# Kernel optimization log

Measured on AMD Instinct MI355X. Metric: run time of the kernel, lower is better.

The kernel has to match this reference:

```python
import jax, jax.numpy as jnp
import numpy as np

NEG_SLOPE = 0.2
EPS = 1e-6


def setup_inputs() -> dict:
    key = jax.random.key(0)
    k1, k2 = jax.random.split(key)
    B, C, N = 4, 64, 32768
    x = jax.random.normal(k1, (B, C, 3, N), dtype=jnp.float32)
    # VNLinear weight: nn.Linear(in, out, bias=False).weight -> [out, in]
    W = jax.random.normal(k2, (C, C), dtype=jnp.float32) * (1.0 / np.sqrt(C))
    return {"x": x, "W": W}


def reference(x, W):
    # VNLinear: kron(W, eye(3)) conv2d == per-3-vector channel mix
    # d[b,o,v,n] = sum_i W[o,i] * x[b,i,v,n]
    d = jnp.einsum('oi,bivn->bovn', W, x)
    dotprod = jnp.sum(x * d, axis=2, keepdims=True)      # [B,C,1,N]
    d_norm_sq = jnp.sum(d * d, axis=2, keepdims=True)    # [B,C,1,N]
    neg = x - (1.0 - NEG_SLOPE) * (dotprod / (d_norm_sq + EPS)) * d
    return jnp.where(dotprod >= 0, x, neg)
```

## Files before the change

kernel.cpp:

```cpp
#include <hip/hip_runtime.h>

#define NEG_SLOPE 0.2f
#define EPS 1e-6f


#define C_CH 64
#define V_DIM 3
#define N_FULL 32768
#define NT 64
#define THREADS 512

typedef __attribute__((ext_vector_type(8))) short bf16x8;
typedef __attribute__((ext_vector_type(4))) float f32x4;

__device__ __forceinline__ ushort f2bf(float f) {
    union { float f; unsigned u; } v; v.f = f;
    unsigned r = v.u + 0x7FFFu + ((v.u >> 16) & 1u);
    return (ushort)(r >> 16);
}
__device__ __forceinline__ float bf2f(ushort s) {
    union { unsigned u; float f; } v; v.u = ((unsigned)s) << 16; return v.f;
}
__device__ __forceinline__ unsigned pack_hl(float x) {
    union { float f; unsigned u; } a; a.f = x;
    unsigned t0 = a.u + 0x8000u;
    union { unsigned u; float f; } hb; hb.u = t0 & 0xffff0000u;
    union { float f; unsigned u; } rb; rb.f = x - hb.f;
    return __builtin_amdgcn_perm(t0, rb.u, 0x07060302u);
}
__device__ __forceinline__ float u2f(unsigned u) {
    union { unsigned u; float f; } v; v.u = u; return v.f;
}

__device__ __forceinline__ int swz(int row) { return ((row >> 3) & 3) << 4; }

__global__ __launch_bounds__(THREADS, 4)
void vn_mfma64(const float* __restrict__ x,
               const float* __restrict__ Wf,
               float* __restrict__ out) {
    __shared__ unsigned xs[V_DIM * C_CH][NT];

    const int t    = threadIdx.x;
    const int tile = blockIdx.x;
    const int b    = tile >> 9;
    const int n0   = (tile & 511) << 6;

    const float* xb = x + (size_t)b * (C_CH * V_DIM * N_FULL) + n0;

    const int lane = t & 63;
    const int w    = t >> 6;
    const int wo   = w >> 2;
    const int wn   = w & 3;
    const int l4   = lane & 15;
    const int hi   = lane >> 4;

    float4 xr[6];
    #pragma unroll
    for (int it = 0; it < 6; ++it) {
        int idx = t + it * THREADS;
        int r   = idx >> 4;
        int c4  = (idx & 15) << 2;
        xr[it] = *(const float4*)(xb + (size_t)r * N_FULL + c4);
    }

    bf16x8 Ah[2][2], Al[2][2];
    #pragma unroll
    for (int m = 0; m < 2; ++m)
        #pragma unroll
        for (int kh = 0; kh < 2; ++kh) {
            const float* wp = Wf + (size_t)(wo * 32 + m * 16 + l4) * C_CH + kh * 32 + hi * 8;
            float4 wa = *(const float4*)wp;
            float4 wb = *(const float4*)(wp + 4);
            float wf[8] = {wa.x, wa.y, wa.z, wa.w, wb.x, wb.y, wb.z, wb.w};
            bf16x8 h, l;
            #pragma unroll
            for (int j = 0; j < 8; ++j) {
                ushort hb = f2bf(wf[j]);
                h[j] = (short)hb;
                l[j] = (short)f2bf(wf[j] - bf2f(hb));
            }
            Ah[m][kh] = h; Al[m][kh] = l;
        }

    #pragma unroll
    for (int it = 0; it < 6; ++it) {
        int idx = t + it * THREADS;
        int r   = idx >> 4;
        int c4  = (idx & 15) << 2;
        int i   = (r * 171) >> 9;
        int v   = r - 3 * i;
        int rowp = v * 64 + i;
        unsigned p[4] = {pack_hl(xr[it].x), pack_hl(xr[it].y),
                         pack_hl(xr[it].z), pack_hl(xr[it].w)};
        *(uint4*)&xs[rowp][c4 ^ swz(rowp)] = *(const uint4*)p;
    }
    __syncthreads();

    f32x4 acc[2][3];
    #pragma unroll
    for (int m = 0; m < 2; ++m)
        #pragma unroll
        for (int v = 0; v < 3; ++v)
            acc[m][v] = (f32x4){0.f, 0.f, 0.f, 0.f};

    const int acol = (wn * 16 + l4) ^ (hi << 4);
    #pragma unroll
    for (int v = 0; v < 3; ++v) {
        #pragma unroll
        for (int kh = 0; kh < 2; ++kh) {
            const int rowb = v * 64 + kh * 32 + hi * 8;
            unsigned p[8];
            #pragma unroll
            for (int j = 0; j < 8; ++j)
                p[j] = xs[rowb + j][acol];
            union { bf16x8 v8; unsigned d[4]; } BH, BL;
            #pragma unroll
            for (int q = 0; q < 4; ++q) {
                BH.d[q] = __builtin_amdgcn_perm(p[2 * q + 1], p[2 * q], 0x07060302u);
                BL.d[q] = __builtin_amdgcn_perm(p[2 * q + 1], p[2 * q], 0x05040100u);
            }
            #pragma unroll
            for (int m = 0; m < 2; ++m) {
                acc[m][v] = __builtin_amdgcn_mfma_f32_16x16x32_bf16(Ah[m][kh], BH.v8, acc[m][v], 0, 0, 0);
                acc[m][v] = __builtin_amdgcn_mfma_f32_16x16x32_bf16(Ah[m][kh], BL.v8, acc[m][v], 0, 0, 0);
                acc[m][v] = __builtin_amdgcn_mfma_f32_16x16x32_bf16(Al[m][kh], BH.v8, acc[m][v], 0, 0, 0);
            }
        }
    }

    const int n = wn * 16 + l4;
    float* ob = out + (size_t)b * (C_CH * V_DIM * N_FULL) + n0 + n;
    #pragma unroll
    for (int m = 0; m < 2; ++m) {
        #pragma unroll
        for (int r = 0; r < 4; ++r) {
            const int o = wo * 32 + m * 16 + hi * 4 + r;
            const int ecol = n ^ (((m * 2 + (hi >> 1)) & 3) << 4);
            float xv[3], dv[3];
            #pragma unroll
            for (int v = 0; v < 3; ++v) {
                unsigned p = xs[v * 64 + o][ecol];
                xv[v] = u2f(p & 0xffff0000u) + u2f(p << 16);
                dv[v] = acc[m][v][r];
            }
            float dot  = xv[0] * dv[0] + xv[1] * dv[1] + xv[2] * dv[2];
            float dnsq = dv[0] * dv[0] + dv[1] * dv[1] + dv[2] * dv[2];
            float f = (1.0f - NEG_SLOPE) * dot * __builtin_amdgcn_rcpf(dnsq + EPS);
            f = (dot >= 0.f) ? 0.f : f;
            float o0 = fmaf(-f, dv[0], xv[0]);
            float o1 = fmaf(-f, dv[1], xv[1]);
            float o2 = fmaf(-f, dv[2], xv[2]);
            float* op = ob + (size_t)o * (V_DIM * N_FULL);
            op[0 * N_FULL] = o0;
            op[1 * N_FULL] = o1;
            op[2 * N_FULL] = o2;
        }
    }
}

extern "C" void kernel_launch(void* const* d_in, const int* in_sizes, int n_in,
                              void* d_out, int out_size, void* d_ws, size_t ws_size,
                              hipStream_t stream) {
    const float* x = (const float*)d_in[0];
    const float* W = (const float*)d_in[1];
    float* out = (float*)d_out;

    const int B = 4;
    const int blocks = B * (N_FULL / NT);
    vn_mfma64<<<blocks, THREADS, 0, stream>>>(x, W, out);
}
```

Before: 42.76 us.

## Process four tiles per block with double-buffered LDS and register prefetch

Each block now walks four 32-column tiles with 256 threads. The next tile's global loads are issued into registers before the current tile's MFMA and epilogue, then packed into a second LDS buffer, so load latency overlaps compute. The aim is to hide memory latency and amortise the W split across tiles. The cost is double LDS use, fewer blocks (1024 versus 2048), narrower 128-byte row segments per load, and a lower occupancy hint.

```diff
diff --git a/kernel.cpp b/kernel.cpp
--- a/kernel.cpp
+++ b/kernel.cpp
@@ -7,8 +7,9 @@
 #define C_CH 64
 #define V_DIM 3
 #define N_FULL 32768
-#define NT 64
-#define THREADS 512
+#define NT 32
+#define THREADS 256
+#define TPB 4
 
 typedef __attribute__((ext_vector_type(8))) short bf16x8;
 typedef __attribute__((ext_vector_type(4))) float f32x4;
@@ -32,35 +33,36 @@
     union { unsigned u; float f; } v; v.u = u; return v.f;
 }
 
-__device__ __forceinline__ int swz(int row) { return ((row >> 3) & 3) << 4; }
-
-__global__ __launch_bounds__(THREADS, 4)
-void vn_mfma64(const float* __restrict__ x,
-               const float* __restrict__ Wf,
-               float* __restrict__ out) {
-    __shared__ unsigned xs[V_DIM * C_CH][NT];
-
-    const int t    = threadIdx.x;
-    const int tile = blockIdx.x;
-    const int b    = tile >> 9;
-    const int n0   = (tile & 511) << 6;
-
-    const float* xb = x + (size_t)b * (C_CH * V_DIM * N_FULL) + n0;
+__device__ __forceinline__ int swz(int row) { return ((row >> 3) & 1) << 4; }
+
+__global__ __launch_bounds__(THREADS, 3)
+void vn_pipe(const float* __restrict__ x,
+             const float* __restrict__ Wf,
+             float* __restrict__ out) {
+    __shared__ unsigned xs[2][V_DIM * C_CH][NT];
+
+    const int t     = threadIdx.x;
+    const int tile0 = blockIdx.x * TPB;
+    const int b     = tile0 >> 10;
+    const float* xbase = x   + (size_t)b * (C_CH * V_DIM * N_FULL);
+    float*       obase = out + (size_t)b * (C_CH * V_DIM * N_FULL);
 
     const int lane = t & 63;
     const int w    = t >> 6;
-    const int wo   = w >> 2;
-    const int wn   = w & 3;
+    const int wo   = w >> 1;
+    const int wn   = w & 1;
     const int l4   = lane & 15;
     const int hi   = lane >> 4;
 
+
     float4 xr[6];
-    #pragma unroll
-    for (int it = 0; it < 6; ++it) {
-        int idx = t + it * THREADS;
-        int r   = idx >> 4;
-        int c4  = (idx & 15) << 2;
-        xr[it] = *(const float4*)(xb + (size_t)r * N_FULL + c4);
+    {
+        const float* xb = xbase + ((tile0 & 1023) << 5);
+        #pragma unroll
+        for (int it = 0; it < 6; ++it) {
+            int idx = t + it * THREADS;
+            xr[it] = *(const float4*)(xb + (size_t)(idx >> 3) * N_FULL + ((idx & 7) << 2));
+        }
     }
 
     bf16x8 Ah[2][2], Al[2][2];
@@ -85,76 +87,108 @@
     #pragma unroll
     for (int it = 0; it < 6; ++it) {
         int idx = t + it * THREADS;
-        int r   = idx >> 4;
-        int c4  = (idx & 15) << 2;
+        int r   = idx >> 3;
+        int c4  = (idx & 7) << 2;
         int i   = (r * 171) >> 9;
         int v   = r - 3 * i;
         int rowp = v * 64 + i;
         unsigned p[4] = {pack_hl(xr[it].x), pack_hl(xr[it].y),
                          pack_hl(xr[it].z), pack_hl(xr[it].w)};
-        *(uint4*)&xs[rowp][c4 ^ swz(rowp)] = *(const uint4*)p;
+        *(uint4*)&xs[0][rowp][c4 ^ swz(rowp)] = *(const uint4*)p;
     }
     __syncthreads();
 
-    f32x4 acc[2][3];
+    const int acol = (wn * 16 + l4) ^ ((hi & 1) << 4);
+    const int n    = wn * 16 + l4;
+    const int ecol = n ^ ((hi >> 1) << 4);
+
     #pragma unroll
-    for (int m = 0; m < 2; ++m)
-        #pragma unroll
-        for (int v = 0; v < 3; ++v)
-            acc[m][v] = (f32x4){0.f, 0.f, 0.f, 0.f};
-
-    const int acol = (wn * 16 + l4) ^ (hi << 4);
-    #pragma unroll
-    for (int v = 0; v < 3; ++v) {
-        #pragma unroll
-        for (int kh = 0; kh < 2; ++kh) {
-            const int rowb = v * 64 + kh * 32 + hi * 8;
-            unsigned p[8];
-            #pragma unroll
-            for (int j = 0; j < 8; ++j)
-                p[j] = xs[rowb + j][acol];
-            union { bf16x8 v8; unsigned d[4]; } BH, BL;
-            #pragma unroll
-            for (int q = 0; q < 4; ++q) {
-                BH.d[q] = __builtin_amdgcn_perm(p[2 * q + 1], p[2 * q], 0x07060302u);
-                BL.d[q] = __builtin_amdgcn_perm(p[2 * q + 1], p[2 * q], 0x05040100u);
-            }
-            #pragma unroll
-            for (int m = 0; m < 2; ++m) {
-                acc[m][v] = __builtin_amdgcn_mfma_f32_16x16x32_bf16(Ah[m][kh], BH.v8, acc[m][v], 0, 0, 0);
-                acc[m][v] = __builtin_amdgcn_mfma_f32_16x16x32_bf16(Ah[m][kh], BL.v8, acc[m][v], 0, 0, 0);
-                acc[m][v] = __builtin_amdgcn_mfma_f32_16x16x32_bf16(Al[m][kh], BH.v8, acc[m][v], 0, 0, 0);
-            }
-        }
-    }
-
-    const int n = wn * 16 + l4;
-    float* ob = out + (size_t)b * (C_CH * V_DIM * N_FULL) + n0 + n;
-    #pragma unroll
-    for (int m = 0; m < 2; ++m) {
-        #pragma unroll
-        for (int r = 0; r < 4; ++r) {
-            const int o = wo * 32 + m * 16 + hi * 4 + r;
-            const int ecol = n ^ (((m * 2 + (hi >> 1)) & 3) << 4);
-            float xv[3], dv[3];
-            #pragma unroll
-            for (int v = 0; v < 3; ++v) {
-                unsigned p = xs[v * 64 + o][ecol];
-                xv[v] = u2f(p & 0xffff0000u) + u2f(p << 16);
-                dv[v] = acc[m][v][r];
-            }
-            float dot  = xv[0] * dv[0] + xv[1] * dv[1] + xv[2] * dv[2];
-            float dnsq = dv[0] * dv[0] + dv[1] * dv[1] + dv[2] * dv[2];
-            float f = (1.0f - NEG_SLOPE) * dot * __builtin_amdgcn_rcpf(dnsq + EPS);
-            f = (dot >= 0.f) ? 0.f : f;
-            float o0 = fmaf(-f, dv[0], xv[0]);
-            float o1 = fmaf(-f, dv[1], xv[1]);
-            float o2 = fmaf(-f, dv[2], xv[2]);
-            float* op = ob + (size_t)o * (V_DIM * N_FULL);
-            op[0 * N_FULL] = o0;
-            op[1 * N_FULL] = o1;
-            op[2 * N_FULL] = o2;
-        }
+    for (int tt = 0; tt < TPB; ++tt) {
+        const int cur = tt & 1;
+        const int n0c = ((tile0 + tt) & 1023) << 5;
+
+        if (tt + 1 < TPB) {
+            const float* xb = xbase + (((tile0 + tt + 1) & 1023) << 5);
+            #pragma unroll
+            for (int it = 0; it < 6; ++it) {
+                int idx = t + it * THREADS;
+                xr[it] = *(const float4*)(xb + (size_t)(idx >> 3) * N_FULL + ((idx & 7) << 2));
+            }
+        }
+
+        f32x4 acc[2][3];
+        #pragma unroll
+        for (int m = 0; m < 2; ++m)
+            #pragma unroll
+            for (int v = 0; v < 3; ++v)
+                acc[m][v] = (f32x4){0.f, 0.f, 0.f, 0.f};
+
+        #pragma unroll
+        for (int v = 0; v < 3; ++v) {
+            #pragma unroll
+            for (int kh = 0; kh < 2; ++kh) {
+                const int rowb = v * 64 + kh * 32 + hi * 8;
+                unsigned p[8];
+                #pragma unroll
+                for (int j = 0; j < 8; ++j)
+                    p[j] = xs[cur][rowb + j][acol];
+                union { bf16x8 v8; unsigned d[4]; } BH, BL;
+                #pragma unroll
+                for (int q = 0; q < 4; ++q) {
+                    BH.d[q] = __builtin_amdgcn_perm(p[2 * q + 1], p[2 * q], 0x07060302u);
+                    BL.d[q] = __builtin_amdgcn_perm(p[2 * q + 1], p[2 * q], 0x05040100u);
+                }
+                #pragma unroll
+                for (int m = 0; m < 2; ++m) {
+                    acc[m][v] = __builtin_amdgcn_mfma_f32_16x16x32_bf16(Ah[m][kh], BH.v8, acc[m][v], 0, 0, 0);
+                    acc[m][v] = __builtin_amdgcn_mfma_f32_16x16x32_bf16(Ah[m][kh], BL.v8, acc[m][v], 0, 0, 0);
+                    acc[m][v] = __builtin_amdgcn_mfma_f32_16x16x32_bf16(Al[m][kh], BH.v8, acc[m][v], 0, 0, 0);
+                }
+            }
+        }
+
+        float* ob = obase + n0c + n;
+        #pragma unroll
+        for (int m = 0; m < 2; ++m) {
+            #pragma unroll
+            for (int rr = 0; rr < 4; ++rr) {
+                const int o = wo * 32 + m * 16 + hi * 4 + rr;
+                float xv[3], dv[3];
+                #pragma unroll
+                for (int v = 0; v < 3; ++v) {
+                    unsigned p = xs[cur][v * 64 + o][ecol];
+                    xv[v] = u2f(p & 0xffff0000u) + u2f(p << 16);
+                    dv[v] = acc[m][v][rr];
+                }
+                float dot  = xv[0] * dv[0] + xv[1] * dv[1] + xv[2] * dv[2];
+                float dnsq = dv[0] * dv[0] + dv[1] * dv[1] + dv[2] * dv[2];
+                float f = (1.0f - NEG_SLOPE) * dot * __builtin_amdgcn_rcpf(dnsq + EPS);
+                f = (dot >= 0.f) ? 0.f : f;
+                float o0 = fmaf(-f, dv[0], xv[0]);
+                float o1 = fmaf(-f, dv[1], xv[1]);
+                float o2 = fmaf(-f, dv[2], xv[2]);
+                float* op = ob + (size_t)o * (V_DIM * N_FULL);
+                op[0 * N_FULL] = o0;
+                op[1 * N_FULL] = o1;
+                op[2 * N_FULL] = o2;
+            }
+        }
+
+        if (tt + 1 < TPB) {
+            #pragma unroll
+            for (int it = 0; it < 6; ++it) {
+                int idx = t + it * THREADS;
+                int r   = idx >> 3;
+                int c4  = (idx & 7) << 2;
+                int i   = (r * 171) >> 9;
+                int v   = r - 3 * i;
+                int rowp = v * 64 + i;
+                unsigned p[4] = {pack_hl(xr[it].x), pack_hl(xr[it].y),
+                                 pack_hl(xr[it].z), pack_hl(xr[it].w)};
+                *(uint4*)&xs[cur ^ 1][rowp][c4 ^ swz(rowp)] = *(const uint4*)p;
+            }
+        }
+        __syncthreads();
     }
 }
 
@@ -166,6 +200,6 @@
     float* out = (float*)d_out;
 
     const int B = 4;
-    const int blocks = B * (N_FULL / NT);
-    vn_mfma64<<<blocks, THREADS, 0, stream>>>(x, W, out);
-}
+    const int blocks = B * (N_FULL / NT) / TPB;
+    vn_pipe<<<blocks, THREADS, 0, stream>>>(x, W, out);
+}
```

New measurement: 38.69 us. -9.5%, faster.
